# Kernel tuning notes

Measured on AMD Instinct MI355X. Metric: run time of the kernel, lower is better.

The kernel has to match this reference:

```python
import jax, jax.numpy as jnp
import numpy as np

EPS = 1e-6

def _layernorm(x):
    mu = jnp.mean(x, axis=-1, keepdims=True)
    var = jnp.mean(jnp.square(x - mu), axis=-1, keepdims=True)
    return (x - mu) / jnp.sqrt(var + EPS)

def setup_inputs() -> dict:
    key = jax.random.key(0)
    ks = jax.random.split(key, 12)
    B, N, C = 4, 1024, 1024
    H = 16
    Dff = 4 * C
    s = 0.02
    x = jax.random.normal(ks[0], (B, N, C), dtype=jnp.float32)
    mask = jax.random.randint(ks[1], (N, N), 0, 2) > 0  # True = attend
    wq = jax.random.normal(ks[2], (C, C), dtype=jnp.float32) * s
    bq = jnp.zeros((C,), dtype=jnp.float32)
    wkv = jax.random.normal(ks[3], (C, 2 * C), dtype=jnp.float32) * s
    bkv = jnp.zeros((2 * C,), dtype=jnp.float32)
    wo = jax.random.normal(ks[4], (C, C), dtype=jnp.float32) * s
    bo = jnp.zeros((C,), dtype=jnp.float32)
    w1 = jax.random.normal(ks[5], (C, Dff), dtype=jnp.float32) * s
    b1 = jnp.zeros((Dff,), dtype=jnp.float32)
    w2 = jax.random.normal(ks[6], (Dff, C), dtype=jnp.float32) * s
    b2 = jnp.zeros((C,), dtype=jnp.float32)
    return {"x": x, "mask": mask, "wq": wq, "bq": bq, "wkv": wkv, "bkv": bkv,
            "wo": wo, "bo": bo, "w1": w1, "b1": b1, "w2": w2, "b2": b2}

def reference(x, mask, wq, bq, wkv, bkv, wo, bo, w1, b1, w2, b2):
    B, N, C = x.shape
    H = 16
    d = C // H
    scale = d ** -0.5
    max_neg = -jnp.finfo(x.dtype).max
    # attn_bias: 0 where mask True, -max where False; broadcast [1,1,N,N]
    attn_bias = jnp.where(mask, jnp.asarray(0.0, x.dtype), jnp.asarray(max_neg, x.dtype))[None, None]

    # --- pre-norm attention ---
    xn = _layernorm(x)
    q = (xn @ wq + bq).reshape(B, N, H, d)
    kv = xn @ wkv + bkv
    k, v = jnp.split(kv, 2, axis=-1)
    k = k.reshape(B, N, H, d)
    v = v.reshape(B, N, H, d)
    sim = jnp.einsum('bihd,bjhd->bhij', q, k) * scale + attn_bias
    attn = jax.nn.softmax(sim, axis=-1)
    o = jnp.einsum('bhij,bjhd->bihd', attn, v).reshape(B, N, C)
    x = x + (o @ wo + bo)

    # --- pre-norm MLP with tanh-approx GELU ---
    xn = _layernorm(x)
    h = jax.nn.gelu(xn @ w1 + b1, approximate=True)
    x = x + (h @ w2 + b2)
    return x
```

## Files before the change

kernel.cpp:

```cpp
#include <hip/hip_runtime.h>
#include <hip/hip_bf16.h>

typedef short bf16x8 __attribute__((ext_vector_type(8)));
typedef float f32x4 __attribute__((ext_vector_type(4)));
typedef unsigned short u16x8 __attribute__((ext_vector_type(8)));

#define MFMA16(a,b,c) __builtin_amdgcn_mfma_f32_16x16x32_bf16((a),(b),(c),0,0,0)

__device__ inline unsigned short f32_to_bf16(float f){
  union { float f; unsigned u; } v; v.f = f;
  unsigned u = v.u;
  u += 0x7FFFu + ((u >> 16) & 1u);
  return (unsigned short)(u >> 16);
}
__device__ inline float bf16_to_f32(unsigned short u){
  union { unsigned u; float f; } v; v.u = ((unsigned)u)<<16; return v.f;
}

__device__ inline float gelu_tanh(float x){
  float x3 = x*x*x;
  float t = tanhf(0.7978845608028654f*(x + 0.044715f*x3));
  return 0.5f*x*(1.0f+t);
}

__device__ inline void gload16(const void* g, void* l){
  __builtin_amdgcn_global_load_lds(
      (const __attribute__((address_space(1))) void*)g,
      (__attribute__((address_space(3))) void*)l, 16, 0, 0);
}

__device__ inline int xcd_swz(int lin, int nwg){
  int cpx = nwg >> 3;
  return (lin & 7)*cpx + (lin >> 3);
}

__global__ void detect_mask_kernel(const unsigned* __restrict__ m, int* __restrict__ flag){
  __shared__ int s;
  if (threadIdx.x == 0) s = 0;
  __syncthreads();
  unsigned w = m[threadIdx.x];
  if (w > 1u) atomicOr(&s, 1);
  __syncthreads();
  if (threadIdx.x == 0) *flag = s;
}

__global__ __launch_bounds__(256) void mask_bias_kernel(
    const void* __restrict__ mask, const int* __restrict__ flag,
    unsigned short* __restrict__ biasr){
  __shared__ float mt[16][64];
  int qg = blockIdx.x, jt = blockIdx.y;
  int t = threadIdx.x;
  int fl = *flag;
  int jc = jt*64 + (t&63);
  #pragma unroll
  for (int k2=0;k2<4;k2++){
    int qr = qg*16 + (t>>6) + k2*4;
    bool a = fl ? (((const unsigned char*)mask)[(size_t)qr*1024 + jc] != 0)
                : (((const int*)mask)[(size_t)qr*1024 + jc] != 0);
    mt[(t>>6)+k2*4][t&63] = a ? -23.083120654223414f : -1e30f;
  }
  __syncthreads();
  ushort4 ob;
  unsigned short tmp[4];
  #pragma unroll
  for (int u=0;u<4;u++){
    int p = t*4+u;
    int e = p&15, lane = p>>4;
    int i = e>>2, jj = e&3;
    int ln2 = lane&15, g2 = lane>>4;
    tmp[u] = f32_to_bf16(mt[g2*4+i][jj*16+ln2]);
  }
  ob.x=tmp[0]; ob.y=tmp[1]; ob.z=tmp[2]; ob.w=tmp[3];
  *(ushort4*)&biasr[((size_t)(qg*16+jt)*64)*16 + t*4] = ob;
}

__global__ __launch_bounds__(256) void transpose_cvt_kernel(
    const float* __restrict__ W, unsigned short* __restrict__ WT, int K, int N){
  __shared__ float tile[32][37];
  int n0 = blockIdx.x*32, k0 = blockIdx.y*32;
  int r = threadIdx.x>>3, c4 = threadIdx.x&7;
  float4 v = *(const float4*)&W[(size_t)(k0+r)*N + n0 + c4*4];
  tile[r][c4*4+0]=v.x; tile[r][c4*4+1]=v.y; tile[r][c4*4+2]=v.z; tile[r][c4*4+3]=v.w;
  __syncthreads();
  ushort4 o;
  o.x = f32_to_bf16(tile[c4*4+0][r]);
  o.y = f32_to_bf16(tile[c4*4+1][r]);
  o.z = f32_to_bf16(tile[c4*4+2][r]);
  o.w = f32_to_bf16(tile[c4*4+3][r]);
  *(ushort4*)&WT[(size_t)(n0+r)*K + k0 + c4*4] = o;
}

__global__ __launch_bounds__(256) void vtrans_kernel(
    const unsigned short* __restrict__ qkv, unsigned short* __restrict__ vt){
  __shared__ unsigned short t[32][33];
  int b = blockIdx.z;
  int n0 = blockIdx.x*32, d0 = blockIdx.y*32;
  int tx = threadIdx.x & 31, ty = threadIdx.x >> 5;
  #pragma unroll
  for (int r=0;r<4;r++)
    t[ty+8*r][tx] = qkv[(size_t)(b*1024 + n0+ty+8*r)*3072 + 2048 + d0+tx];
  __syncthreads();
  #pragma unroll
  for (int r=0;r<4;r++)
    vt[((size_t)b<<20) + (size_t)(d0+ty+8*r)*1024 + n0+tx] = t[tx][ty+8*r];
}

__global__ void bias_concat_kernel(const float* __restrict__ bq,
                                   const float* __restrict__ bkv,
                                   float* __restrict__ dst){
  int i = blockIdx.x*256 + threadIdx.x;
  if (i < 3072) dst[i] = (i < 1024) ? bq[i] : bkv[i-1024];
}

__global__ __launch_bounds__(256) void ln_kernel(const float* __restrict__ x,
                                                 unsigned short* __restrict__ xn){
  const int C = 1024;
  size_t row = blockIdx.x;
  float4 v = reinterpret_cast<const float4*>(x + row*C)[threadIdx.x];
  float s = v.x+v.y+v.z+v.w;
  float q = v.x*v.x+v.y*v.y+v.z*v.z+v.w*v.w;
  #pragma unroll
  for (int off=32; off; off>>=1){ s += __shfl_xor(s,off); q += __shfl_xor(q,off); }
  __shared__ float sm[8];
  int wv = threadIdx.x>>6, ln = threadIdx.x&63;
  if (ln==0){ sm[wv]=s; sm[4+wv]=q; }
  __syncthreads();
  float S = sm[0]+sm[1]+sm[2]+sm[3];
  float Q = sm[4]+sm[5]+sm[6]+sm[7];
  float mu  = S*(1.0f/1024.0f);
  float var = Q*(1.0f/1024.0f) - mu*mu;
  float inv = rsqrtf(var + 1e-6f);
  ushort4 o;
  o.x = f32_to_bf16((v.x-mu)*inv);
  o.y = f32_to_bf16((v.y-mu)*inv);
  o.z = f32_to_bf16((v.z-mu)*inv);
  o.w = f32_to_bf16((v.w-mu)*inv);
  reinterpret_cast<ushort4*>(xn + row*C)[threadIdx.x] = o;
}

template<int EPI>
__global__ __launch_bounds__(256) void gemm64_kernel(
    const unsigned short* __restrict__ A,
    const unsigned short* __restrict__ BT,
    const float* __restrict__ bias,
    const float* __restrict__ resid,
    void* __restrict__ Cout,
    int M, int N, int K)
{
  __shared__ __align__(16) unsigned short lA[3][128*32];
  __shared__ __align__(16) unsigned short lB[3][64*32];
  int tid = threadIdx.x, wave = tid>>6, lane = tid&63;
  int nbx = gridDim.x;
  int lin = blockIdx.y*nbx + blockIdx.x;
  int w = xcd_swz(lin, nbx*gridDim.y);
  int m0 = (w/nbx)*128, n0 = (w%nbx)*64;
  int ln = lane&15, g = lane>>4;

  int srow = wave*16 + (lane>>2);
  int scol = (lane&3)*8;
  const unsigned short* gA0 = A  + (size_t)(m0+srow)*K    + scol;
  const unsigned short* gA1 = A  + (size_t)(m0+64+srow)*K + scol;
  const unsigned short* gB0 = BT + (size_t)(n0+srow)*K    + scol;
  int lof0 = wave*512;
  int lof1 = 64*32 + wave*512;

  f32x4 acc[4][2] = {};
  int wm = wave>>1, wn = wave&1;
  int nt = K/32;

  auto STAGE = [&](int t, int buf){
    int ko = t*32;
    gload16(gA0+ko, &lA[buf][lof0]);
    gload16(gA1+ko, &lA[buf][lof1]);
    gload16(gB0+ko, &lB[buf][lof0]);
  };

  STAGE(0,0); STAGE(1,1); STAGE(2,2);

  int cb = 0;
  for (int t=0; t<nt; ++t){
    int rem = nt-1-t;
    if (rem >= 2)      asm volatile("s_waitcnt vmcnt(6)" ::: "memory");
    else if (rem == 1) asm volatile("s_waitcnt vmcnt(3)" ::: "memory");
    else               asm volatile("s_waitcnt vmcnt(0)" ::: "memory");
    __builtin_amdgcn_s_barrier();

    bf16x8 a[4], b[2];
    const unsigned short* pA = &lA[cb][(wm*64+ln)*32 + g*8];
    const unsigned short* pB = &lB[cb][(wn*32+ln)*32 + g*8];
    #pragma unroll
    for (int i=0;i<4;i++) a[i] = *(const bf16x8*)(pA + i*16*32);
    #pragma unroll
    for (int i=0;i<2;i++) b[i] = *(const bf16x8*)(pB + i*16*32);
    #pragma unroll
    for (int mi=0;mi<4;mi++)
      #pragma unroll
      for (int ni=0;ni<2;ni++)
        acc[mi][ni] = MFMA16(a[mi], b[ni], acc[mi][ni]);

    asm volatile("s_waitcnt lgkmcnt(0)" ::: "memory");
    __builtin_amdgcn_s_barrier();
    if (t+3 < nt) STAGE(t+3, cb);
    cb = (cb==2) ? 0 : cb+1;
  }

  #pragma unroll
  for (int mi=0;mi<4;mi++){
    int r0 = m0 + wm*64 + mi*16 + g*4;
    #pragma unroll
    for (int ni=0;ni<2;ni++){
      int c = n0 + wn*32 + ni*16 + ln;
      float bs = bias[c];
      f32x4 cc = acc[mi][ni];
      #pragma unroll
      for (int i=0;i<4;i++){
        int r = r0 + i;
        float v = cc[i] + bs;
        if (EPI == 1){
          v += resid[(size_t)r*N + c];
          ((float*)Cout)[(size_t)r*N + c] = v;
        } else if (EPI == 2){
          ((unsigned short*)Cout)[(size_t)r*N + c] = f32_to_bf16(gelu_tanh(v));
        } else {
          ((unsigned short*)Cout)[(size_t)r*N + c] = f32_to_bf16(v);
        }
      }
    }
  }
}

template<int EPI>
__global__ __launch_bounds__(512) void gemm8_kernel(
    const unsigned short* __restrict__ A,
    const unsigned short* __restrict__ BT,
    const float* __restrict__ bias,
    void* __restrict__ Cout,
    int M, int N, int K)
{
  extern __shared__ __align__(16) char smem[];
  const int tid = threadIdx.x, wave = tid>>6, lane = tid&63;
  const int ln = lane&15, g = lane>>4;
  const int wm = wave>>2, wn = wave&3;
  const int nbx = gridDim.x;
  const int lin = blockIdx.y*nbx + blockIdx.x;
  const int wsw = xcd_swz(lin, nbx*gridDim.y);
  const int m0 = (wsw/nbx)*256, n0 = (wsw%nbx)*256;
  const int NT = K>>6;
  const int axor = (g*16) ^ (((ln>>2)&3)<<4);

  auto STAGE = [&](int kt, int h){
    const bool isB = h&1; const int kh = h>>1;
    const unsigned short* src = isB ? BT : A;
    const int base0 = isB ? n0 : m0;
    char* region = smem + (isB?65536:0) + (kt&1)*32768 + kh*16384;
    #pragma unroll
    for (int r=0;r<2;r++){
      int idx = r*512 + tid;
      int row = idx>>2;
      int col = kt*64 + kh*32 + ((((idx&3)*16) ^ (((row>>2)&3)<<4))>>1);
      gload16(src + (size_t)(base0+row)*K + col,
              region + (r*512 + wave*64)*16);
    }
  };

  STAGE(0,0); STAGE(0,1); STAGE(0,2); STAGE(0,3);
  STAGE(1,0); STAGE(1,1); STAGE(1,2);
  asm volatile("s_waitcnt vmcnt(6)" ::: "memory");
  __builtin_amdgcn_s_barrier();
  __builtin_amdgcn_sched_barrier(0);

  f32x4 acc[8][4] = {};
  bf16x8 a[8], b[2];

  for (int t=0; t<NT; ++t){
    const int cur = t&1;
    char* Ac0 = smem + cur*32768;
    char* Ac1 = Ac0 + 16384;
    char* Bc0 = smem + 65536 + cur*32768;
    char* Bc1 = Bc0 + 16384;
    #pragma unroll
    for (int mi=0;mi<8;mi++)
      a[mi] = *(const bf16x8*)(Ac0 + (wm*128+mi*16+ln)*64 + axor);
    b[0] = *(const bf16x8*)(Bc0 + (wn*64+ 0+ln)*64 + axor);
    b[1] = *(const bf16x8*)(Bc0 + (wn*64+16+ln)*64 + axor);
    if (t+1 < NT) STAGE(t+1,3);
    __builtin_amdgcn_s_barrier();
    __builtin_amdgcn_s_setprio(1);
    #pragma unroll
    for (int mi=0;mi<8;mi++){
      acc[mi][0] = MFMA16(a[mi], b[0], acc[mi][0]);
      acc[mi][1] = MFMA16(a[mi], b[1], acc[mi][1]);
    }
    __builtin_amdgcn_s_setprio(0);
    __builtin_amdgcn_s_barrier();
    b[0] = *(const bf16x8*)(Bc0 + (wn*64+32+ln)*64 + axor);
    b[1] = *(const bf16x8*)(Bc0 + (wn*64+48+ln)*64 + axor);
    if (t+2 < NT) STAGE(t+2,0);
    __builtin_amdgcn_s_barrier();
    __builtin_amdgcn_s_setprio(1);
    #pragma unroll
    for (int mi=0;mi<8;mi++){
      acc[mi][2] = MFMA16(a[mi], b[0], acc[mi][2]);
      acc[mi][3] = MFMA16(a[mi], b[1], acc[mi][3]);
    }
    __builtin_amdgcn_s_setprio(0);
    __builtin_amdgcn_s_barrier();
    #pragma unroll
    for (int mi=0;mi<8;mi++)
      a[mi] = *(const bf16x8*)(Ac1 + (wm*128+mi*16+ln)*64 + axor);
    b[0] = *(const bf16x8*)(Bc1 + (wn*64+ 0+ln)*64 + axor);
    b[1] = *(const bf16x8*)(Bc1 + (wn*64+16+ln)*64 + axor);
    if (t+2 < NT) STAGE(t+2,1);
    __builtin_amdgcn_s_barrier();
    __builtin_amdgcn_s_setprio(1);
    #pragma unroll
    for (int mi=0;mi<8;mi++){
      acc[mi][0] = MFMA16(a[mi], b[0], acc[mi][0]);
      acc[mi][1] = MFMA16(a[mi], b[1], acc[mi][1]);
    }
    __builtin_amdgcn_s_setprio(0);
    __builtin_amdgcn_s_barrier();
    b[0] = *(const bf16x8*)(Bc1 + (wn*64+32+ln)*64 + axor);
    b[1] = *(const bf16x8*)(Bc1 + (wn*64+48+ln)*64 + axor);
    if (t+2 < NT) STAGE(t+2,2);
    __builtin_amdgcn_s_barrier();
    __builtin_amdgcn_s_setprio(1);
    #pragma unroll
    for (int mi=0;mi<8;mi++){
      acc[mi][2] = MFMA16(a[mi], b[0], acc[mi][2]);
      acc[mi][3] = MFMA16(a[mi], b[1], acc[mi][3]);
    }
    __builtin_amdgcn_s_setprio(0);
    if (t+2 < NT) asm volatile("s_waitcnt vmcnt(6)" ::: "memory");
    else          asm volatile("s_waitcnt vmcnt(0)" ::: "memory");
    __builtin_amdgcn_s_barrier();
    __builtin_amdgcn_sched_barrier(0);
  }

  #pragma unroll
  for (int mi=0;mi<8;mi++){
    int r0 = m0 + wm*128 + mi*16 + g*4;
    #pragma unroll
    for (int nj=0;nj<4;nj++){
      int c = n0 + wn*64 + nj*16 + ln;
      float bs = bias[c];
      f32x4 cc = acc[mi][nj];
      #pragma unroll
      for (int i=0;i<4;i++){
        int r = r0 + i;
        float v = cc[i] + bs;
        if (EPI == 2){
          ((unsigned short*)Cout)[(size_t)r*N + c] = f32_to_bf16(gelu_tanh(v));
        } else {
          ((unsigned short*)Cout)[(size_t)r*N + c] = f32_to_bf16(v);
        }
      }
    }
  }
}

__global__ __launch_bounds__(256,6) void attn_kernel(
    const unsigned short* __restrict__ qkv,
    const unsigned short* __restrict__ vt,
    const unsigned short* __restrict__ biasr,
    unsigned short* __restrict__ pn,
    float* __restrict__ lsumg)
{
  const int N = 1024, NK = 3072;
  const float SCL = 0.18033688011112042f;
  __shared__ __align__(16) unsigned short lK[64*64];
  __shared__ __align__(16) unsigned short lV[64*64];
  __shared__ __align__(16) unsigned short plds[4][16][72];
  int bh = blockIdx.x, qt = blockIdx.y, sp = blockIdx.z;
  int b = bh>>4, h = bh&15;
  int tid = threadIdx.x, wave = tid>>6, lane = tid&63;
  int ln = lane&15, g = lane>>4;
  size_t base = (size_t)b*N;
  int q_local = qt*64 + wave*16;

  const unsigned short* qptr = qkv + (base + q_local + ln)*NK + h*64;
  bf16x8 aq0 = *(const bf16x8*)(qptr + g*8);
  bf16x8 aq1 = *(const bf16x8*)(qptr + 32 + g*8);

  int r0s = tid>>3,        c0 = (tid&7) ^ (r0s&7);
  int r1s = 32 + (tid>>3), c1 = (tid&7) ^ (r1s&7);
  const unsigned short* kg0 = qkv + (base + r0s)*NK + 1024 + h*64 + c0*8;
  const unsigned short* kg1 = qkv + (base + r1s)*NK + 1024 + h*64 + c1*8;
  const unsigned short* vg0 = vt + ((size_t)b<<20) + (size_t)(h*64 + r0s)*N + c0*8;
  const unsigned short* vg1 = vt + ((size_t)b<<20) + (size_t)(h*64 + r1s)*N + c1*8;
  char* lKd0 = (char*)lK + (wave*64)*16;
  char* lKd1 = (char*)lK + (256 + wave*64)*16;
  char* lVd0 = (char*)lV + (wave*64)*16;
  char* lVd1 = (char*)lV + (256 + wave*64)*16;

  const unsigned short* brp = biasr +
      (((size_t)(qt*4 + wave)*16)*64 + lane)*16;

  f32x4 oacc[4] = {};
  float lsum[4] = {0.f,0.f,0.f,0.f};
  const int xl = (ln&7);

  for (int t=0; t<8; ++t){
    int j0 = sp*512 + t*64;
    __syncthreads();
    gload16(kg0 + (size_t)j0*NK, lKd0);
    gload16(kg1 + (size_t)j0*NK, lKd1);
    gload16(vg0 + j0, lVd0);
    gload16(vg1 + j0, lVd1);
    int jt = j0>>6;
    bf16x8 bb0 = *(const bf16x8*)(brp + (size_t)jt*1024);
    bf16x8 bb1 = *(const bf16x8*)(brp + (size_t)jt*1024 + 8);
    asm volatile("s_waitcnt vmcnt(0)" ::: "memory");
    __builtin_amdgcn_s_barrier();

    f32x4 s[4];
    #pragma unroll
    for (int jj=0;jj<4;jj++){
      int row = jj*16+ln;
      bf16x8 k0 = *(const bf16x8*)((const char*)lK + row*128 + ((g^xl)<<4));
      bf16x8 k1 = *(const bf16x8*)((const char*)lK + row*128 + (((g+4)^xl)<<4));
      s[jj] = (f32x4){};
      s[jj] = MFMA16(aq0, k0, s[jj]);
      s[jj] = MFMA16(aq1, k1, s[jj]);
    }
    #pragma unroll
    for (int i=0;i<4;i++){
      #pragma unroll
      for (int jj=0;jj<4;jj++){
        int e = i*4+jj;
        unsigned short bu = (e<8) ? (unsigned short)bb0[e] : (unsigned short)bb1[e-8];
        float ev = exp2f(fmaf(s[jj][i], SCL, bf16_to_f32(bu)));
        lsum[i] += ev;
        plds[wave][4*g+i][jj*16+ln] = f32_to_bf16(ev);
      }
    }
    asm volatile("s_waitcnt lgkmcnt(0)" ::: "memory");
    __builtin_amdgcn_sched_barrier(0);
    bf16x8 p0 = *(const bf16x8*)&plds[wave][ln][g*8];
    bf16x8 p1 = *(const bf16x8*)&plds[wave][ln][32 + g*8];
    #pragma unroll
    for (int nd=0;nd<4;nd++){
      int row = nd*16+ln;
      bf16x8 v0 = *(const bf16x8*)((const char*)lV + row*128 + ((g^xl)<<4));
      bf16x8 v1 = *(const bf16x8*)((const char*)lV + row*128 + (((g+4)^xl)<<4));
      oacc[nd] = MFMA16(p0, v0, oacc[nd]);
      oacc[nd] = MFMA16(p1, v1, oacc[nd]);
    }
  }

  #pragma unroll
  for (int i=0;i<4;i++){
    float l = lsum[i];
    l += __shfl_xor(l,1); l += __shfl_xor(l,2);
    l += __shfl_xor(l,4); l += __shfl_xor(l,8);
    if (ln == 0)
      lsumg[((size_t)sp<<16) + (size_t)(base + q_local + 4*g + i)*16 + h] = l;
  }
  #pragma unroll
  for (int nd=0;nd<4;nd++){
    #pragma unroll
    for (int i=0;i<4;i++){
      int qr = q_local + 4*g + i;
      pn[((size_t)sp<<22) + (base+qr)*1024 + h*64 + nd*16 + ln] = f32_to_bf16(oacc[nd][i]);
    }
  }
}

__global__ __launch_bounds__(256) void attn_reduce_kernel(
    const unsigned short* __restrict__ pn,
    const float* __restrict__ lsumg,
    unsigned short* __restrict__ o)
{
  size_t idx = ((size_t)blockIdx.x*256 + threadIdx.x)*8;
  int r = (int)(idx>>10);
  int h = (int)((idx&1023)>>6);
  float inv = 1.0f/(lsumg[(size_t)r*16+h] + lsumg[(1u<<16) + (size_t)r*16+h]);
  u16x8 p0 = *(const u16x8*)(pn + idx);
  u16x8 p1 = *(const u16x8*)(pn + (1u<<22) + idx);
  u16x8 res;
  #pragma unroll
  for (int e=0;e<8;e++)
    res[e] = f32_to_bf16((bf16_to_f32((unsigned short)p0[e]) +
                          bf16_to_f32((unsigned short)p1[e]))*inv);
  *(u16x8*)(o + idx) = res;
}

extern "C" void kernel_launch(void* const* d_in, const int* in_sizes, int n_in,
                              void* d_out, int out_size, void* d_ws, size_t ws_size,
                              hipStream_t stream)
{
  (void)in_sizes; (void)n_in; (void)out_size; (void)ws_size;
  const float* x   = (const float*)d_in[0];
  const void*  mask= d_in[1];
  const float* wq  = (const float*)d_in[2];
  const float* bq  = (const float*)d_in[3];
  const float* wkv = (const float*)d_in[4];
  const float* bkv = (const float*)d_in[5];
  const float* wo  = (const float*)d_in[6];
  const float* bo  = (const float*)d_in[7];
  const float* w1  = (const float*)d_in[8];
  const float* b1  = (const float*)d_in[9];
  const float* w2  = (const float*)d_in[10];
  const float* b2  = (const float*)d_in[11];
  float* out = (float*)d_out;

  char* ws = (char*)d_ws;
  size_t off = 0;
  auto alloc = [&](size_t bytes){ size_t o = off; off += (bytes + 255) & ~(size_t)255; return o; };
  unsigned short* WqkvT = (unsigned short*)(ws + alloc(3072u*1024u*2));
  unsigned short* WoT   = (unsigned short*)(ws + alloc(1024u*1024u*2));
  unsigned short* W1T   = (unsigned short*)(ws + alloc(4096u*1024u*2));
  unsigned short* W2T   = (unsigned short*)(ws + alloc(1024u*4096u*2));
  float*          BIASQ = (float*)(ws + alloc(3072u*4));
  int*            FLAG  = (int*)(ws + alloc(256));
  float*          LSUM  = (float*)(ws + alloc(2u*4096u*16u*4));
  unsigned short* BIASR = (unsigned short*)(ws + alloc(64u*16u*64u*16u*2));
  unsigned short* XN    = (unsigned short*)(ws + alloc(4096u*1024u*2));
  float*          X1    = (float*)(ws + alloc(4096u*1024u*4));
  unsigned short* QKV   = (unsigned short*)(ws + alloc(4096u*4096u*2));
  unsigned short* VT    = QKV + (size_t)4096u*3072u;
  unsigned short* PN    = (unsigned short*)X1;

  hipFuncSetAttribute(reinterpret_cast<const void*>(&gemm8_kernel<0>),
                      hipFuncAttributeMaxDynamicSharedMemorySize, 131072);
  hipFuncSetAttribute(reinterpret_cast<const void*>(&gemm8_kernel<2>),
                      hipFuncAttributeMaxDynamicSharedMemorySize, 131072);

  transpose_cvt_kernel<<<dim3(32,32),  256, 0, stream>>>(wq,  WqkvT,               1024, 1024);
  transpose_cvt_kernel<<<dim3(64,32),  256, 0, stream>>>(wkv, WqkvT + 1024u*1024u, 1024, 2048);
  transpose_cvt_kernel<<<dim3(32,32),  256, 0, stream>>>(wo,  WoT,                 1024, 1024);
  transpose_cvt_kernel<<<dim3(128,32), 256, 0, stream>>>(w1,  W1T,                 1024, 4096);
  transpose_cvt_kernel<<<dim3(32,128), 256, 0, stream>>>(w2,  W2T,                 4096, 1024);
  bias_concat_kernel<<<12, 256, 0, stream>>>(bq, bkv, BIASQ);
  detect_mask_kernel<<<1, 256, 0, stream>>>((const unsigned*)mask, FLAG);
  mask_bias_kernel<<<dim3(64,16), 256, 0, stream>>>(mask, FLAG, BIASR);

  ln_kernel<<<4096, 256, 0, stream>>>(x, XN);
  gemm8_kernel<0><<<dim3(12,16), 512, 131072, stream>>>(XN, WqkvT, BIASQ, QKV, 4096, 3072, 1024);
  vtrans_kernel<<<dim3(32,32,4), 256, 0, stream>>>(QKV, VT);
  attn_kernel<<<dim3(64,16,2), 256, 0, stream>>>(QKV, VT, BIASR, PN, LSUM);
  attn_reduce_kernel<<<2048, 256, 0, stream>>>(PN, LSUM, XN);
  gemm64_kernel<1><<<dim3(16,32), 256, 0, stream>>>(XN, WoT, bo, x, X1, 4096, 1024, 1024);
  ln_kernel<<<4096, 256, 0, stream>>>(X1, XN);
  gemm8_kernel<2><<<dim3(16,16), 512, 131072, stream>>>(XN, W1T, b1, QKV, 4096, 4096, 1024);
  gemm64_kernel<1><<<dim3(16,32), 256, 0, stream>>>(QKV, W2T, b2, X1, out, 4096, 1024, 4096);
}
```

Baseline: 269.4 us.

## Split-K the output-projection and down-projection GEMMs with atomic accumulation

Replaces the 128x64-tile GEMM used for the Wo and W2 projections with a split-K variant: the K dimension is split into 2 or 4 slices across blockIdx.z, and each slice atomically adds its partial tile into an output prefilled with residual plus bias by a new init kernel. This multiplies the block count from 512 to 1024/2048 to fill more CUs and shortens each block's serial K loop. In exchange it adds an extra elementwise pass over the output, scattered fp32 atomics per element, and summation order that is no longer deterministic.

```diff
diff --git a/kernel.cpp b/kernel.cpp
--- a/kernel.cpp
+++ b/kernel.cpp
@@ -110,6 +110,16 @@
                                    float* __restrict__ dst){
   int i = blockIdx.x*256 + threadIdx.x;
   if (i < 3072) dst[i] = (i < 1024) ? bq[i] : bkv[i-1024];
+}
+
+__global__ __launch_bounds__(256) void init_out_kernel(
+    const float* __restrict__ resid, const float* __restrict__ bias,
+    float* __restrict__ out){
+  size_t i = (size_t)blockIdx.x*256 + threadIdx.x;
+  float4 r = ((const float4*)resid)[i];
+  float4 b = ((const float4*)bias)[i & 255];
+  float4 o; o.x=r.x+b.x; o.y=r.y+b.y; o.z=r.z+b.z; o.w=r.w+b.w;
+  ((float4*)out)[i] = o;
 }
 
 __global__ __launch_bounds__(256) void ln_kernel(const float* __restrict__ x,
@@ -138,13 +148,11 @@
   reinterpret_cast<ushort4*>(xn + row*C)[threadIdx.x] = o;
 }
 
-template<int EPI>
-__global__ __launch_bounds__(256) void gemm64_kernel(
+template<int SPLITS>
+__global__ __launch_bounds__(256) void gemm_sk_kernel(
     const unsigned short* __restrict__ A,
     const unsigned short* __restrict__ BT,
-    const float* __restrict__ bias,
-    const float* __restrict__ resid,
-    void* __restrict__ Cout,
+    float* __restrict__ Cout,
     int M, int N, int K)
 {
   __shared__ __align__(16) unsigned short lA[3][128*32];
@@ -154,19 +162,20 @@
   int lin = blockIdx.y*nbx + blockIdx.x;
   int w = xcd_swz(lin, nbx*gridDim.y);
   int m0 = (w/nbx)*128, n0 = (w%nbx)*64;
+  int kbase = blockIdx.z * (K/SPLITS);
   int ln = lane&15, g = lane>>4;
 
   int srow = wave*16 + (lane>>2);
   int scol = (lane&3)*8;
-  const unsigned short* gA0 = A  + (size_t)(m0+srow)*K    + scol;
-  const unsigned short* gA1 = A  + (size_t)(m0+64+srow)*K + scol;
-  const unsigned short* gB0 = BT + (size_t)(n0+srow)*K    + scol;
+  const unsigned short* gA0 = A  + (size_t)(m0+srow)*K    + kbase + scol;
+  const unsigned short* gA1 = A  + (size_t)(m0+64+srow)*K + kbase + scol;
+  const unsigned short* gB0 = BT + (size_t)(n0+srow)*K    + kbase + scol;
   int lof0 = wave*512;
   int lof1 = 64*32 + wave*512;
 
   f32x4 acc[4][2] = {};
   int wm = wave>>1, wn = wave&1;
-  int nt = K/32;
+  int nt = (K/SPLITS)/32;
 
   auto STAGE = [&](int t, int buf){
     int ko = t*32;
@@ -210,21 +219,10 @@
     #pragma unroll
     for (int ni=0;ni<2;ni++){
       int c = n0 + wn*32 + ni*16 + ln;
-      float bs = bias[c];
       f32x4 cc = acc[mi][ni];
       #pragma unroll
-      for (int i=0;i<4;i++){
-        int r = r0 + i;
-        float v = cc[i] + bs;
-        if (EPI == 1){
-          v += resid[(size_t)r*N + c];
-          ((float*)Cout)[(size_t)r*N + c] = v;
-        } else if (EPI == 2){
-          ((unsigned short*)Cout)[(size_t)r*N + c] = f32_to_bf16(gelu_tanh(v));
-        } else {
-          ((unsigned short*)Cout)[(size_t)r*N + c] = f32_to_bf16(v);
-        }
-      }
+      for (int i=0;i<4;i++)
+        atomicAdd(&Cout[(size_t)(r0+i)*N + c], cc[i]);
     }
   }
 }
@@ -540,8 +538,10 @@
   vtrans_kernel<<<dim3(32,32,4), 256, 0, stream>>>(QKV, VT);
   attn_kernel<<<dim3(64,16,2), 256, 0, stream>>>(QKV, VT, BIASR, PN, LSUM);
   attn_reduce_kernel<<<2048, 256, 0, stream>>>(PN, LSUM, XN);
-  gemm64_kernel<1><<<dim3(16,32), 256, 0, stream>>>(XN, WoT, bo, x, X1, 4096, 1024, 1024);
+  init_out_kernel<<<4096, 256, 0, stream>>>(x, bo, X1);
+  gemm_sk_kernel<2><<<dim3(16,32,2), 256, 0, stream>>>(XN, WoT, X1, 4096, 1024, 1024);
   ln_kernel<<<4096, 256, 0, stream>>>(X1, XN);
   gemm8_kernel<2><<<dim3(16,16), 512, 131072, stream>>>(XN, W1T, b1, QKV, 4096, 4096, 1024);
-  gemm64_kernel<1><<<dim3(16,32), 256, 0, stream>>>(QKV, W2T, b2, X1, out, 4096, 1024, 4096);
-}
+  init_out_kernel<<<4096, 256, 0, stream>>>(X1, b2, out);
+  gemm_sk_kernel<4><<<dim3(16,32,4), 256, 0, stream>>>(QKV, W2T, out, 4096, 1024, 4096);
+}
```

After: 324.5 us. 1.2x slower.
